# Performance work log

Hardware: AMD Instinct MI355X
Metric: run time of the kernel (lower is better)

## Reference

```python
import jax, jax.numpy as jnp
import numpy as np

N_CELLS, N_GENES, N_EDGES, D = 10000, 2000, 4000000, 64


def setup_inputs() -> dict:
    key = jax.random.key(0)
    ks = jax.random.split(key, 10)
    return {
        "c_feat": jax.random.normal(ks[0], (N_CELLS, D), dtype=jnp.float32),
        "g_feat": jax.random.normal(ks[1], (N_GENES, D), dtype=jnp.float32),
        "cs_factor": jax.random.uniform(ks[2], (N_CELLS, 1), dtype=jnp.float32),
        "gs_factor": jax.random.uniform(ks[3], (N_GENES, 1), dtype=jnp.float32),
        "src": jax.random.randint(ks[4], (N_EDGES,), 0, N_CELLS),
        "dst": jax.random.randint(ks[5], (N_EDGES,), 0, N_GENES),
        "Wm": jax.random.normal(ks[6], (D, 1), dtype=jnp.float32) / np.sqrt(D),
        "bm": jnp.zeros((1,), dtype=jnp.float32),
        "Wd": jax.random.normal(ks[7], (D, 1), dtype=jnp.float32) / np.sqrt(D),
        "bd": jnp.zeros((1,), dtype=jnp.float32),
        "Wp": jax.random.normal(ks[8], (D, 1), dtype=jnp.float32) / np.sqrt(D),
        "bp": jnp.zeros((1,), dtype=jnp.float32),
    }


def reference(c_feat, g_feat, cs_factor, gs_factor, src, dst, Wm, bm, Wd, bd, Wp, bp):
    # Per-edge gather + elementwise product: u_mul_v('h','h','h_d')  -> [E, D]
    h_d = c_feat[src] * g_feat[dst]
    # Per-edge broadcast of node factors: gs from dst gene, cs from src cell -> [E, 1]
    gs = gs_factor[dst]
    cs = cs_factor[src]
    # Tiny Linear(D,1) heads
    mu_ = jax.nn.sigmoid(h_d @ Wm + bm)          # dec_mean
    disp_ = h_d @ Wd + bd                        # dec_disp
    pi = jax.nn.sigmoid(h_d @ Wp + bp)           # dec_pi
    # ZINB activations with clamping
    disp = jnp.clip(jax.nn.softplus(gs * disp_), 1e-4, 1e4)   # DispAct
    mu = cs * jnp.clip(jnp.exp(gs * mu_) - 1.0, 1e-5, 1e6)    # MeanAct scaled by cs
    return (mu, disp, pi)
```

## Files before the change

kernel.cpp:

```cpp
#include <hip/hip_runtime.h>
#include <hip/hip_bf16.h>
#include <hip/hip_fp16.h>


typedef unsigned int u32;
typedef unsigned short u16;
typedef long long i64;
typedef _Float16 v2h __attribute__((ext_vector_type(2)));

__device__ __forceinline__ float us2f(u16 u) { union { u32 i; float f; } v; v.i = ((u32)u) << 16; return v.f; }
__device__ __forceinline__ float lo2f(u32 u) { union { u32 i; float f; } v; v.i = u << 16; return v.f; }
__device__ __forceinline__ float hi2f(u32 u) { union { u32 i; float f; } v; v.i = u & 0xffff0000u; return v.f; }

union H2 { u32 u; __half2 h; v2h v; };

#if defined(__has_builtin)
#if __has_builtin(__builtin_amdgcn_fdot2)
#define HAS_FDOT2 1
#endif
#endif

#define FLAGS_OFF 200
#define WHALF_B   1024
#define CS32_B    2048
#define GS32_B    42048
#define CHALF_B   50176
#define GHALF_B   1330176
#define WS_NEED   1586176

__global__ __launch_bounds__(256) void zinb_prep_all(
    const void* __restrict__ c, const void* __restrict__ g,
    const void* __restrict__ cs, const void* __restrict__ gsp,
    const void* __restrict__ src, const void* __restrict__ dst,
    const void* __restrict__ Wm, const void* __restrict__ bm,
    const void* __restrict__ Wd, const void* __restrict__ bd,
    const void* __restrict__ Wp, const void* __restrict__ bp,
    char* __restrict__ wsb, int nc, int ng, int ncs, int ngs, int E)
{
    __shared__ int sf[12];
    int t = threadIdx.x;
    if (t < 12) sf[t] = 0;
    __syncthreads();

    {
        int bad;
        const u32* pc = (const u32*)c;
        bad = 0; for (int i = t; i < 1024; i += 256) { int ex = (pc[i] >> 7) & 0xFF; if (ex >= 135) bad = 1; }
        if (bad) atomicOr(&sf[0], 1);
        const u32* pg = (const u32*)g;
        bad = 0; for (int i = t; i < 1024; i += 256) { int ex = (pg[i] >> 7) & 0xFF; if (ex >= 135) bad = 1; }
        if (bad) atomicOr(&sf[1], 1);
        const u32* ps = (const u32*)cs;
        bad = 0; for (int i = t; i < 1024; i += 256) { int ex = (ps[i] >> 7) & 0xFF; if (ex >= 135) bad = 1; }
        if (bad) atomicOr(&sf[2], 1);
        const u32* pq = (const u32*)gsp;
        bad = 0; for (int i = t; i < 1000; i += 256) { int ex = (pq[i] >> 7) & 0xFF; if (ex >= 135) bad = 1; }
        if (bad) atomicOr(&sf[3], 1);
        const u32* p4 = (const u32*)src;
        int on = 0, en = 0;
        for (int i = t; i < 1024; i += 256) { if (p4[2 * i + 1] != 0) on = 1; if (p4[2 * i] != 0) en = 1; }
        if (on) atomicOr(&sf[4], 1);
        if (en) atomicOr(&sf[5], 1);
        const u32* p5 = (const u32*)dst;
        on = 0; en = 0;
        for (int i = t; i < 1024; i += 256) { if (p5[2 * i + 1] != 0) on = 1; if (p5[2 * i] != 0) en = 1; }
        if (on) atomicOr(&sf[6], 1);
        if (en) atomicOr(&sf[7], 1);
        if (t < 3) {
            const u32* pw = (t == 0) ? (const u32*)Wm : (t == 1) ? (const u32*)Wd : (const u32*)Wp;
            bad = 0; for (int i = 0; i < 32; ++i) { int ex = (pw[i] >> 7) & 0xFF; if (ex >= 135) bad = 1; }
            if (bad) atomicOr(&sf[8 + t], 1);
        }
    }
    __syncthreads();
    int fc = sf[0], fg = sf[1], fcs = sf[2], fgs = sf[3];

    int i = blockIdx.x * 256 + t;
    __half* ch  = (__half*)(wsb + CHALF_B);
    __half* gh  = (__half*)(wsb + GHALF_B);
    float* cs32 = (float*)(wsb + CS32_B);
    float* gs32 = (float*)(wsb + GS32_B);
    if (i < nc) ch[i] = __float2half(fc ? ((const float*)c)[i] : us2f(((const u16*)c)[i]));
    if (i < ng) gh[i] = __float2half(fg ? ((const float*)g)[i] : us2f(((const u16*)g)[i]));
    if (i < ncs) cs32[i] = fcs ? ((const float*)cs)[i] : us2f(((const u16*)cs)[i]);
    if (i < ngs) gs32[i] = fgs ? ((const float*)gsp)[i] : us2f(((const u16*)gsp)[i]);

    if (blockIdx.x == 0) {
        float* W32 = (float*)wsb;
        int w0 = sf[8], w1 = sf[9], w2 = sf[10];
        if (t < 64) {
            W32[t]       = w0 ? ((const float*)Wm)[t] : us2f(((const u16*)Wm)[t]);
            W32[64 + t]  = w1 ? ((const float*)Wd)[t] : us2f(((const u16*)Wd)[t]);
            W32[128 + t] = w2 ? ((const float*)Wp)[t] : us2f(((const u16*)Wp)[t]);
        } else if (t == 64) {
            W32[192] = w0 ? ((const float*)bm)[0] : us2f(((const u16*)bm)[0]);
            W32[193] = w1 ? ((const float*)bd)[0] : us2f(((const u16*)bd)[0]);
            W32[194] = w2 ? ((const float*)bp)[0] : us2f(((const u16*)bp)[0]);
        }
        __syncthreads();
        __half* wh = (__half*)(wsb + WHALF_B);
        if (t < 192) wh[t] = __float2half(W32[t]);
        if (t == 192) {
            int* flg = (int*)wsb + FLAGS_OFF;
            flg[0] = fc; flg[1] = fg; flg[2] = fcs; flg[3] = fgs;
            flg[4] = (!sf[4] && sf[5]) ? 1 : 0;
            flg[5] = (!sf[6] && sf[7]) ? 1 : 0;
        }
    }
}

__global__ __launch_bounds__(256) void zinb_fast2(
    const __half* __restrict__ cT, const __half* __restrict__ gT,
    const float* __restrict__ cs32, const float* __restrict__ gs32,
    const void* __restrict__ src, const void* __restrict__ dst,
    const char* __restrict__ wsb, float* __restrict__ out, int E)
{
    const float* W32 = (const float*)wsb;
    const int* flags = (const int*)wsb + FLAGS_OFF;
    int fs64 = flags[4], fd64 = flags[5];

    int tid = threadIdx.x;
    int q = tid >> 2, l = tid & 3;
    int base = blockIdx.x * 256;

    const uint4* Wh = (const uint4*)(wsb + WHALF_B);
    uint4 m0 = Wh[l],      m1 = Wh[4 + l];
    uint4 d0 = Wh[8 + l],  d1 = Wh[12 + l];
    uint4 p0 = Wh[16 + l], p1 = Wh[20 + l];
    u32 wm[8] = {m0.x, m0.y, m0.z, m0.w, m1.x, m1.y, m1.z, m1.w};
    u32 wd[8] = {d0.x, d0.y, d0.z, d0.w, d1.x, d1.y, d1.z, d1.w};
    u32 wp[8] = {p0.x, p0.y, p0.z, p0.w, p1.x, p1.y, p1.z, p1.w};
    float bmv = W32[192], bdv = W32[193], bpv = W32[194];

    float Sm = 0.f, Sd = 0.f, Sp = 0.f;
    int ss = 0, sd2 = 0, se = -1;

    #pragma unroll
    for (int it = 0; it < 4; ++it) {
        int e = base + it * 64 + q;
        bool ok = (e < E);
        int s = 0, d = 0;
        float am = 0.f, ad = 0.f, ap = 0.f;
        if (ok) {
            s = fs64 ? (int)((const i64*)src)[e] : ((const int*)src)[e];
            d = fd64 ? (int)((const i64*)dst)[e] : ((const int*)dst)[e];
            const uint4* cr = (const uint4*)(cT + (size_t)s * 64);
            const uint4* gr = (const uint4*)(gT + (size_t)d * 64);
            uint4 c0 = cr[l], c1 = cr[4 + l];
            uint4 g0 = gr[l], g1 = gr[4 + l];
            u32 cw[8] = {c0.x, c0.y, c0.z, c0.w, c1.x, c1.y, c1.z, c1.w};
            u32 gw[8] = {g0.x, g0.y, g0.z, g0.w, g1.x, g1.y, g1.z, g1.w};
            #pragma unroll
            for (int j = 0; j < 8; ++j) {
                H2 a, b, pr, w;
                a.u = cw[j]; b.u = gw[j];
                pr.h = __hmul2(a.h, b.h);
#ifdef HAS_FDOT2
                w.u = wm[j]; am = __builtin_amdgcn_fdot2(pr.v, w.v, am, false);
                w.u = wd[j]; ad = __builtin_amdgcn_fdot2(pr.v, w.v, ad, false);
                w.u = wp[j]; ap = __builtin_amdgcn_fdot2(pr.v, w.v, ap, false);
#else
                float2 pf = __half22float2(pr.h);
                H2 t0, t1, t2; t0.u = wm[j]; t1.u = wd[j]; t2.u = wp[j];
                float2 wmf = __half22float2(t0.h);
                float2 wdf = __half22float2(t1.h);
                float2 wpf = __half22float2(t2.h);
                am = fmaf(pf.x, wmf.x, fmaf(pf.y, wmf.y, am));
                ad = fmaf(pf.x, wdf.x, fmaf(pf.y, wdf.y, ad));
                ap = fmaf(pf.x, wpf.x, fmaf(pf.y, wpf.y, ap));
#endif
            }
        }
        am += __shfl_xor(am, 1); am += __shfl_xor(am, 2);
        ad += __shfl_xor(ad, 1); ad += __shfl_xor(ad, 2);
        ap += __shfl_xor(ap, 1); ap += __shfl_xor(ap, 2);
        if (l == it && ok) { Sm = am; Sd = ad; Sp = ap; ss = s; sd2 = d; se = e; }
    }

    if (se >= 0) {
        float cs = cs32[ss];
        float gs = gs32[sd2];
        float mu_ = __builtin_amdgcn_rcpf(1.f + __expf(-(Sm + bmv)));
        float pi  = __builtin_amdgcn_rcpf(1.f + __expf(-(Sp + bpv)));
        float xd  = gs * (Sd + bdv);
        float sp  = fmaxf(xd, 0.f) + __logf(1.f + __expf(-fabsf(xd)));
        float disp = fminf(fmaxf(sp, 1e-4f), 1e4f);
        float em  = __expf(gs * mu_) - 1.f;
        float mu  = cs * fminf(fmaxf(em, 1e-5f), 1e6f);
        out[se]         = mu;
        out[E + se]     = disp;
        out[2 * E + se] = pi;
    }
}

__global__ void zinb_detect(const void* c, int nc, const void* g, int ng,
                            const void* cs, int ncs, const void* gsp, int ngs,
                            const void* src, int ns, const void* dst, int nd,
                            int* flags) {
    __shared__ int s_a, s_b;
    int b = blockIdx.x, t = threadIdx.x;
    if (t == 0) { s_a = 0; s_b = 0; }
    __syncthreads();
    if (b < 4) {
        const u32* p; int n;
        if (b == 0)      { p = (const u32*)c;   n = nc;  }
        else if (b == 1) { p = (const u32*)g;   n = ng;  }
        else if (b == 2) { p = (const u32*)cs;  n = ncs; }
        else             { p = (const u32*)gsp; n = ngs; }
        int words = n / 2; if (words > 16384) words = 16384;
        int bad = 0;
        for (int i = t; i < words; i += 256) { int ex = (p[i] >> 7) & 0xFF; if (ex >= 135) bad = 1; }
        if (bad) atomicOr(&s_a, 1);
        __syncthreads();
        if (t == 0) flags[b] = s_a;
    } else {
        const u32* p = (b == 4) ? (const u32*)src : (const u32*)dst;
        int n = (b == 4) ? ns : nd;
        int pairs = (n < 4096) ? n / 2 : 2048;
        int oddnz = 0, evennz = 0;
        for (int i = t; i < pairs; i += 256) {
            if (p[2 * i + 1] != 0) oddnz = 1;
            if (p[2 * i] != 0)     evennz = 1;
        }
        if (oddnz)  atomicOr(&s_a, 1);
        if (evennz) atomicOr(&s_b, 1);
        __syncthreads();
        if (t == 0) flags[b] = (!s_a && s_b) ? 1 : 0;
    }
}

__global__ void zinb_prep_w(const void* Wm, const void* bm, const void* Wd,
                            const void* bd, const void* Wp, const void* bp,
                            float* W) {
    __shared__ int wf[3];
    int t = threadIdx.x;
    if (t < 3) {
        const u32* p = (t == 0) ? (const u32*)Wm : (t == 1) ? (const u32*)Wd : (const u32*)Wp;
        int bad = 0;
        for (int i = 0; i < 32; ++i) { int ex = (p[i] >> 7) & 0xFF; if (ex >= 135) bad = 1; }
        wf[t] = bad;
    }
    __syncthreads();
    if (t < 64) {
        W[t]       = wf[0] ? ((const float*)Wm)[t] : us2f(((const u16*)Wm)[t]);
        W[64 + t]  = wf[1] ? ((const float*)Wd)[t] : us2f(((const u16*)Wd)[t]);
        W[128 + t] = wf[2] ? ((const float*)Wp)[t] : us2f(((const u16*)Wp)[t]);
    } else if (t == 64) {
        W[192] = wf[0] ? ((const float*)bm)[0] : us2f(((const u16*)bm)[0]);
        W[193] = wf[1] ? ((const float*)bd)[0] : us2f(((const u16*)bd)[0]);
        W[194] = wf[2] ? ((const float*)bp)[0] : us2f(((const u16*)bp)[0]);
    }
}

__global__ __launch_bounds__(256) void zinb_main(
    const void* __restrict__ c_feat, const void* __restrict__ g_feat,
    const void* __restrict__ cs_f, const void* __restrict__ gs_f,
    const void* __restrict__ src, const void* __restrict__ dst,
    const float* __restrict__ W, float* __restrict__ out, int E)
{
    int e = blockIdx.x * 256 + threadIdx.x;
    if (e >= E) return;
    const int* flags = (const int*)W + FLAGS_OFF;
    int fc = flags[0], fg = flags[1], fcs = flags[2], fgs = flags[3];
    int fs64 = flags[4], fd64 = flags[5];
    int s = fs64 ? (int)((const i64*)src)[e] : ((const int*)src)[e];
    int d = fd64 ? (int)((const i64*)dst)[e] : ((const int*)dst)[e];
    const char* crow = (const char*)c_feat + (size_t)s * (fc ? 256 : 128);
    const char* grow = (const char*)g_feat + (size_t)d * (fg ? 256 : 128);
    float accm = 0.f, accd = 0.f, accp = 0.f;
    for (int ch = 0; ch < 4; ++ch) {
        float cb[16], gb[16];
        if (fc) {
            const float4* qq = (const float4*)crow;
            #pragma unroll
            for (int j4 = 0; j4 < 4; ++j4) {
                float4 v = qq[ch * 4 + j4];
                cb[j4 * 4] = v.x; cb[j4 * 4 + 1] = v.y; cb[j4 * 4 + 2] = v.z; cb[j4 * 4 + 3] = v.w;
            }
        } else {
            const uint4* qq = (const uint4*)crow;
            #pragma unroll
            for (int j2 = 0; j2 < 2; ++j2) {
                uint4 v = qq[ch * 2 + j2];
                u32 w[4] = {v.x, v.y, v.z, v.w};
                #pragma unroll
                for (int j = 0; j < 4; ++j) {
                    cb[j2 * 8 + j * 2] = lo2f(w[j]); cb[j2 * 8 + j * 2 + 1] = hi2f(w[j]);
                }
            }
        }
        if (fg) {
            const float4* qq = (const float4*)grow;
            #pragma unroll
            for (int j4 = 0; j4 < 4; ++j4) {
                float4 v = qq[ch * 4 + j4];
                gb[j4 * 4] = v.x; gb[j4 * 4 + 1] = v.y; gb[j4 * 4 + 2] = v.z; gb[j4 * 4 + 3] = v.w;
            }
        } else {
            const uint4* qq = (const uint4*)grow;
            #pragma unroll
            for (int j2 = 0; j2 < 2; ++j2) {
                uint4 v = qq[ch * 2 + j2];
                u32 w[4] = {v.x, v.y, v.z, v.w};
                #pragma unroll
                for (int j = 0; j < 4; ++j) {
                    gb[j2 * 8 + j * 2] = lo2f(w[j]); gb[j2 * 8 + j * 2 + 1] = hi2f(w[j]);
                }
            }
        }
        #pragma unroll
        for (int j = 0; j < 16; ++j) {
            int k = ch * 16 + j;
            float h = cb[j] * gb[j];
            accm = fmaf(h, W[k], accm);
            accd = fmaf(h, W[64 + k], accd);
            accp = fmaf(h, W[128 + k], accp);
        }
    }
    float cs = fcs ? ((const float*)cs_f)[s] : us2f(((const u16*)cs_f)[s]);
    float gs = fgs ? ((const float*)gs_f)[d] : us2f(((const u16*)gs_f)[d]);
    float bmv = W[192], bdv = W[193], bpv = W[194];
    float mu_ = 1.f / (1.f + expf(-(accm + bmv)));
    float pi  = 1.f / (1.f + expf(-(accp + bpv)));
    float xd  = gs * (accd + bdv);
    float sp  = fmaxf(xd, 0.f) + log1pf(expf(-fabsf(xd)));
    float disp = fminf(fmaxf(sp, 1e-4f), 1e4f);
    float em  = expf(gs * mu_) - 1.f;
    float mu  = cs * fminf(fmaxf(em, 1e-5f), 1e6f);
    out[e] = mu; out[E + e] = disp; out[2 * E + e] = pi;
}

extern "C" void kernel_launch(void* const* d_in, const int* in_sizes, int n_in,
                              void* d_out, int out_size, void* d_ws, size_t ws_size,
                              hipStream_t stream) {
    const void* c_feat = d_in[0];
    const void* g_feat = d_in[1];
    const void* cs_f   = d_in[2];
    const void* gs_f   = d_in[3];
    const void* src    = d_in[4];
    const void* dst    = d_in[5];
    const void* Wm     = d_in[6];
    const void* bm     = d_in[7];
    const void* Wd     = d_in[8];
    const void* bd     = d_in[9];
    const void* Wp     = d_in[10];
    const void* bp     = d_in[11];

    int E = in_sizes[4];
    int nc = in_sizes[0], ng = in_sizes[1], ncs = in_sizes[2], ngs = in_sizes[3];
    char* wsb = (char*)d_ws;

    if (ws_size >= (size_t)WS_NEED) {
        int nmax = nc > ng ? nc : ng;
        int prep_blocks = (nmax + 255) / 256;
        zinb_prep_all<<<prep_blocks, 256, 0, stream>>>(
            c_feat, g_feat, cs_f, gs_f, src, dst,
            Wm, bm, Wd, bd, Wp, bp, wsb, nc, ng, ncs, ngs, E);
        int blocks = (E + 255) / 256;
        zinb_fast2<<<blocks, 256, 0, stream>>>(
            (const __half*)(wsb + CHALF_B), (const __half*)(wsb + GHALF_B),
            (const float*)(wsb + CS32_B), (const float*)(wsb + GS32_B),
            src, dst, wsb, (float*)d_out, E);
    } else {
        float* W = (float*)d_ws;
        int* flags = (int*)W + FLAGS_OFF;
        zinb_detect<<<6, 256, 0, stream>>>(c_feat, nc, g_feat, ng, cs_f, ncs,
                                           gs_f, ngs, src, E, dst, in_sizes[5], flags);
        zinb_prep_w<<<1, 256, 0, stream>>>(Wm, bm, Wd, bd, Wp, bp, W);
        int blocks = (E + 255) / 256;
        zinb_main<<<blocks, 256, 0, stream>>>(c_feat, g_feat, cs_f, gs_f, src, dst,
                                              W, (float*)d_out, E);
    }
}
```

Before: 198.5 us.

## Prefetch next edge rows, hoist index loads, use DPP quad reductions

The main kernel is split into a bounds-check-free full-block kernel and a separate tail kernel. The full-block kernel loads all four src/dst indices and the cs/gs factors up front, and software-pipelines the gathers so the next edge's feature rows are fetched while the current one is computed. Shuffle-based quad reductions are replaced with DPP moves. This is meant to hide gather latency and cut shuffle cost, at the price of more registers and a second launch when E is not a multiple of 256.

```diff
diff --git a/kernel.cpp b/kernel.cpp
--- a/kernel.cpp
+++ b/kernel.cpp
@@ -19,6 +19,13 @@
 #define HAS_FDOT2 1
 #endif
 #endif
+
+__device__ __forceinline__ float qadd(float x) {
+    int a = __builtin_amdgcn_mov_dpp(__float_as_int(x), 0xB1, 0xF, 0xF, true);
+    float s = x + __int_as_float(a);
+    int b = __builtin_amdgcn_mov_dpp(__float_as_int(s), 0x4E, 0xF, 0xF, true);
+    return s + __int_as_float(b);
+}
 
 #define FLAGS_OFF 200
 #define WHALF_B   1024
@@ -41,7 +48,6 @@
     int t = threadIdx.x;
     if (t < 12) sf[t] = 0;
     __syncthreads();
-
     {
         int bad;
         const u32* pc = (const u32*)c;
@@ -109,7 +115,52 @@
     }
 }
 
-__global__ __launch_bounds__(256) void zinb_fast2(
+__device__ __forceinline__ void slice_dot(const uint4& c0, const uint4& c1,
+                                          const uint4& g0, const uint4& g1,
+                                          const u32* wm, const u32* wd, const u32* wp,
+                                          float& am, float& ad, float& ap) {
+    u32 cw[8] = {c0.x, c0.y, c0.z, c0.w, c1.x, c1.y, c1.z, c1.w};
+    u32 gw[8] = {g0.x, g0.y, g0.z, g0.w, g1.x, g1.y, g1.z, g1.w};
+    am = 0.f; ad = 0.f; ap = 0.f;
+    #pragma unroll
+    for (int j = 0; j < 8; ++j) {
+        H2 a, b, pr, w;
+        a.u = cw[j]; b.u = gw[j];
+        pr.h = __hmul2(a.h, b.h);
+#ifdef HAS_FDOT2
+        w.u = wm[j]; am = __builtin_amdgcn_fdot2(pr.v, w.v, am, false);
+        w.u = wd[j]; ad = __builtin_amdgcn_fdot2(pr.v, w.v, ad, false);
+        w.u = wp[j]; ap = __builtin_amdgcn_fdot2(pr.v, w.v, ap, false);
+#else
+        float2 pf = __half22float2(pr.h);
+        H2 t0, t1, t2; t0.u = wm[j]; t1.u = wd[j]; t2.u = wp[j];
+        float2 wmf = __half22float2(t0.h);
+        float2 wdf = __half22float2(t1.h);
+        float2 wpf = __half22float2(t2.h);
+        am = fmaf(pf.x, wmf.x, fmaf(pf.y, wmf.y, am));
+        ad = fmaf(pf.x, wdf.x, fmaf(pf.y, wdf.y, ad));
+        ap = fmaf(pf.x, wpf.x, fmaf(pf.y, wpf.y, ap));
+#endif
+    }
+}
+
+__device__ __forceinline__ void zinb_epilogue(float Sm, float Sd, float Sp,
+                                              float cs, float gs,
+                                              float bmv, float bdv, float bpv,
+                                              float* out, int E, int e) {
+    float mu_ = __builtin_amdgcn_rcpf(1.f + __expf(-(Sm + bmv)));
+    float pi  = __builtin_amdgcn_rcpf(1.f + __expf(-(Sp + bpv)));
+    float xd  = gs * (Sd + bdv);
+    float sp  = fmaxf(xd, 0.f) + __logf(1.f + __expf(-fabsf(xd)));
+    float disp = fminf(fmaxf(sp, 1e-4f), 1e4f);
+    float em  = __expf(gs * mu_) - 1.f;
+    float mu  = cs * fminf(fmaxf(em, 1e-5f), 1e6f);
+    out[e]         = mu;
+    out[E + e]     = disp;
+    out[2 * E + e] = pi;
+}
+
+__global__ __launch_bounds__(256) void zinb_fast3(
     const __half* __restrict__ cT, const __half* __restrict__ gT,
     const float* __restrict__ cs32, const float* __restrict__ gs32,
     const void* __restrict__ src, const void* __restrict__ dst,
@@ -122,6 +173,70 @@
     int tid = threadIdx.x;
     int q = tid >> 2, l = tid & 3;
     int base = blockIdx.x * 256;
+
+    int sI[4], dI[4];
+    #pragma unroll
+    for (int it = 0; it < 4; ++it) {
+        int e = base + it * 64 + q;
+        sI[it] = fs64 ? (int)((const i64*)src)[e] : ((const int*)src)[e];
+        dI[it] = fd64 ? (int)((const i64*)dst)[e] : ((const int*)dst)[e];
+    }
+    int s_own = sI[0], d_own = dI[0];
+    #pragma unroll
+    for (int it = 1; it < 4; ++it) {
+        if (l == it) { s_own = sI[it]; d_own = dI[it]; }
+    }
+    float cs = cs32[s_own];
+    float gs = gs32[d_own];
+
+    const uint4* Wh = (const uint4*)(wsb + WHALF_B);
+    uint4 m0 = Wh[l],      m1 = Wh[4 + l];
+    uint4 d0 = Wh[8 + l],  d1 = Wh[12 + l];
+    uint4 p0 = Wh[16 + l], p1 = Wh[20 + l];
+    u32 wm[8] = {m0.x, m0.y, m0.z, m0.w, m1.x, m1.y, m1.z, m1.w};
+    u32 wd[8] = {d0.x, d0.y, d0.z, d0.w, d1.x, d1.y, d1.z, d1.w};
+    u32 wp[8] = {p0.x, p0.y, p0.z, p0.w, p1.x, p1.y, p1.z, p1.w};
+    float bmv = W32[192], bdv = W32[193], bpv = W32[194];
+
+    const uint4* cr = (const uint4*)(cT + (size_t)sI[0] * 64);
+    const uint4* gr = (const uint4*)(gT + (size_t)dI[0] * 64);
+    uint4 c0 = cr[l], c1 = cr[4 + l];
+    uint4 g0 = gr[l], g1 = gr[4 + l];
+
+    float Sm = 0.f, Sd = 0.f, Sp = 0.f;
+    #pragma unroll
+    for (int it = 0; it < 4; ++it) {
+        uint4 nc0, nc1, ng0, ng1;
+        if (it < 3) {
+            const uint4* crn = (const uint4*)(cT + (size_t)sI[it + 1] * 64);
+            const uint4* grn = (const uint4*)(gT + (size_t)dI[it + 1] * 64);
+            nc0 = crn[l]; nc1 = crn[4 + l];
+            ng0 = grn[l]; ng1 = grn[4 + l];
+        }
+        float am, ad, ap;
+        slice_dot(c0, c1, g0, g1, wm, wd, wp, am, ad, ap);
+        am = qadd(am); ad = qadd(ad); ap = qadd(ap);
+        if (l == it) { Sm = am; Sd = ad; Sp = ap; }
+        if (it < 3) { c0 = nc0; c1 = nc1; g0 = ng0; g1 = ng1; }
+    }
+
+    int e_own = base + l * 64 + q;
+    zinb_epilogue(Sm, Sd, Sp, cs, gs, bmv, bdv, bpv, out, E, e_own);
+}
+
+__global__ __launch_bounds__(256) void zinb_fast2t(
+    const __half* __restrict__ cT, const __half* __restrict__ gT,
+    const float* __restrict__ cs32, const float* __restrict__ gs32,
+    const void* __restrict__ src, const void* __restrict__ dst,
+    const char* __restrict__ wsb, float* __restrict__ out, int E, int base0)
+{
+    const float* W32 = (const float*)wsb;
+    const int* flags = (const int*)wsb + FLAGS_OFF;
+    int fs64 = flags[4], fd64 = flags[5];
+
+    int tid = threadIdx.x;
+    int q = tid >> 2, l = tid & 3;
+    int base = base0 + blockIdx.x * 256;
 
     const uint4* Wh = (const uint4*)(wsb + WHALF_B);
     uint4 m0 = Wh[l],      m1 = Wh[4 + l];
@@ -148,49 +263,14 @@
             const uint4* gr = (const uint4*)(gT + (size_t)d * 64);
             uint4 c0 = cr[l], c1 = cr[4 + l];
             uint4 g0 = gr[l], g1 = gr[4 + l];
-            u32 cw[8] = {c0.x, c0.y, c0.z, c0.w, c1.x, c1.y, c1.z, c1.w};
-            u32 gw[8] = {g0.x, g0.y, g0.z, g0.w, g1.x, g1.y, g1.z, g1.w};
-            #pragma unroll
-            for (int j = 0; j < 8; ++j) {
-                H2 a, b, pr, w;
-                a.u = cw[j]; b.u = gw[j];
-                pr.h = __hmul2(a.h, b.h);
-#ifdef HAS_FDOT2
-                w.u = wm[j]; am = __builtin_amdgcn_fdot2(pr.v, w.v, am, false);
-                w.u = wd[j]; ad = __builtin_amdgcn_fdot2(pr.v, w.v, ad, false);
-                w.u = wp[j]; ap = __builtin_amdgcn_fdot2(pr.v, w.v, ap, false);
-#else
-                float2 pf = __half22float2(pr.h);
-                H2 t0, t1, t2; t0.u = wm[j]; t1.u = wd[j]; t2.u = wp[j];
-                float2 wmf = __half22float2(t0.h);
-                float2 wdf = __half22float2(t1.h);
-                float2 wpf = __half22float2(t2.h);
-                am = fmaf(pf.x, wmf.x, fmaf(pf.y, wmf.y, am));
-                ad = fmaf(pf.x, wdf.x, fmaf(pf.y, wdf.y, ad));
-                ap = fmaf(pf.x, wpf.x, fmaf(pf.y, wpf.y, ap));
-#endif
-            }
-        }
-        am += __shfl_xor(am, 1); am += __shfl_xor(am, 2);
-        ad += __shfl_xor(ad, 1); ad += __shfl_xor(ad, 2);
-        ap += __shfl_xor(ap, 1); ap += __shfl_xor(ap, 2);
+            slice_dot(c0, c1, g0, g1, wm, wd, wp, am, ad, ap);
+        }
+        am = qadd(am); ad = qadd(ad); ap = qadd(ap);
         if (l == it && ok) { Sm = am; Sd = ad; Sp = ap; ss = s; sd2 = d; se = e; }
     }
 
-    if (se >= 0) {
-        float cs = cs32[ss];
-        float gs = gs32[sd2];
-        float mu_ = __builtin_amdgcn_rcpf(1.f + __expf(-(Sm + bmv)));
-        float pi  = __builtin_amdgcn_rcpf(1.f + __expf(-(Sp + bpv)));
-        float xd  = gs * (Sd + bdv);
-        float sp  = fmaxf(xd, 0.f) + __logf(1.f + __expf(-fabsf(xd)));
-        float disp = fminf(fmaxf(sp, 1e-4f), 1e4f);
-        float em  = __expf(gs * mu_) - 1.f;
-        float mu  = cs * fminf(fmaxf(em, 1e-5f), 1e6f);
-        out[se]         = mu;
-        out[E + se]     = disp;
-        out[2 * E + se] = pi;
-    }
+    if (se >= 0)
+        zinb_epilogue(Sm, Sd, Sp, cs32[ss], gs32[sd2], bmv, bdv, bpv, out, E, se);
 }
 
 __global__ void zinb_detect(const void* c, int nc, const void* g, int ng,
@@ -356,11 +436,20 @@
         zinb_prep_all<<<prep_blocks, 256, 0, stream>>>(
             c_feat, g_feat, cs_f, gs_f, src, dst,
             Wm, bm, Wd, bd, Wp, bp, wsb, nc, ng, ncs, ngs, E);
-        int blocks = (E + 255) / 256;
-        zinb_fast2<<<blocks, 256, 0, stream>>>(
-            (const __half*)(wsb + CHALF_B), (const __half*)(wsb + GHALF_B),
-            (const float*)(wsb + CS32_B), (const float*)(wsb + GS32_B),
-            src, dst, wsb, (float*)d_out, E);
+
+        const __half* cT = (const __half*)(wsb + CHALF_B);
+        const __half* gT = (const __half*)(wsb + GHALF_B);
+        const float* cs32 = (const float*)(wsb + CS32_B);
+        const float* gs32 = (const float*)(wsb + GS32_B);
+
+        int full_blocks = E / 256;
+        if (full_blocks > 0)
+            zinb_fast3<<<full_blocks, 256, 0, stream>>>(cT, gT, cs32, gs32, src, dst,
+                                                        wsb, (float*)d_out, E);
+        int tail = E - full_blocks * 256;
+        if (tail > 0)
+            zinb_fast2t<<<1, 256, 0, stream>>>(cT, gT, cs32, gs32, src, dst,
+                                               wsb, (float*)d_out, E, full_blocks * 256);
     } else {
         float* W = (float*)d_ws;
         int* flags = (int*)W + FLAGS_OFF;
```

Measured after the change: 195.3 us. Within noise of the previous version (-1.6%).
